# Kernel tuning notes

Measured on AMD Instinct MI355X. Metric: run time of the kernel, lower is better.

## Reference

```python
import jax, jax.numpy as jnp
import numpy as np

CAP = 15.0
EPS = 1e-6
NUM_HEADS = 16
HEAD_DIM = 64

def _rmsnorm(x, w):
    xf = x.astype(jnp.float32)
    var = jnp.mean(xf * xf, axis=-1, keepdims=True)
    return w * (xf * jax.lax.rsqrt(var + EPS)).astype(x.dtype)

def _gate(g):
    # sigmoid(soft_cap(g)) with cap 15
    return jax.nn.sigmoid(CAP * jnp.tanh(g / CAP))

def setup_inputs() -> dict:
    key = jax.random.key(0)
    ks = jax.random.split(key, 4)
    B, S, D = 4, 2048, 1024
    H, Dh = NUM_HEADS, HEAD_DIM
    return {
        "x": jax.random.normal(ks[0], (B, S, D), jnp.float32),
        "hidden_state": jnp.zeros((B, H, Dh, Dh), jnp.float32),
        "w_rms": jnp.ones((D,), jnp.float32),
        "w_qkv": jax.random.normal(ks[1], (D, 3 * H * Dh), jnp.float32) * 0.02,
        "w_gate": jax.random.normal(ks[2], (D, 3 * H), jnp.float32) * 0.02,
        "w_out": jax.random.normal(ks[3], (D, D), jnp.float32) * 0.02,
    }

def reference(x, hidden_state, w_rms, w_qkv, w_gate, w_out):
    B, S, D = x.shape
    H, Dh = NUM_HEADS, HEAD_DIM
    residual = x
    xn = _rmsnorm(x, w_rms)
    qkv = (xn @ w_qkv).reshape(B, S, 3, H, Dh)
    q, k, v = qkv[:, :, 0], qkv[:, :, 1], qkv[:, :, 2]  # [B,S,H,Dh]
    gates = _gate((xn @ w_gate).reshape(B, S, 3, H))
    i_g, f_g, o_g = gates[:, :, 0], gates[:, :, 1], gates[:, :, 2]  # [B,S,H]

    # time-major for scan: [S,B,H,...]
    def tm(a):
        return jnp.moveaxis(a, 1, 0)

    def step(state, inp):
        qt, kt, vt, it, ft, ot = inp  # [B,H,Dh]/[B,H]
        kv = kt[..., :, None] * vt[..., None, :]            # [B,H,Dh,Dh]
        state = ft[..., None, None] * state + it[..., None, None] * kv
        h = jnp.einsum('bhd,bhde->bhe', qt, state) * ot[..., None]
        return state, h

    _, h_seq = jax.lax.scan(step, hidden_state,
                            (tm(q), tm(k), tm(v), tm(i_g), tm(f_g), tm(o_g)))
    out = jnp.moveaxis(h_seq, 0, 1).reshape(B, S, H * Dh) @ w_out
    return residual + out
```

## Files before the change

### kernel.cpp

```cpp
#include <hip/hip_runtime.h>
#include <math.h>

typedef unsigned short u16;
typedef unsigned int   u32;
typedef __bf16 bf16x8 __attribute__((ext_vector_type(8)));
typedef float  f32x4  __attribute__((ext_vector_type(4)));

#define NBATCH 4
#define SEQ    2048
#define DIM    1024
#define NH     16
#define BH     64
#define NC     32
#define ROWS   8192
#define N1     3200

__device__ __forceinline__ u16 f2bf(float f) {
  u32 u = __builtin_bit_cast(u32, f);
  u32 r = u + 0x7fffu + ((u >> 16) & 1u);
  return (u16)(r >> 16);
}
__device__ __forceinline__ float bf2f(u16 h) {
  return __builtin_bit_cast(float, (u32)h << 16);
}

__device__ __forceinline__ void gl2lds16(const u16* g, u16* l) {
  __builtin_amdgcn_global_load_lds(
      (const __attribute__((address_space(1))) u32*)g,
      (__attribute__((address_space(3))) u32*)l, 16, 0, 0);
}

__global__ __launch_bounds__(256) void transpose_w(const float* __restrict__ W,
                                                   u16* __restrict__ Bt, int K, int N) {
  __shared__ float tile[32][33];
  const int n0 = blockIdx.x * 32, k0 = blockIdx.y * 32;
  const int tx = threadIdx.x, ty = threadIdx.y;
  #pragma unroll
  for (int i = 0; i < 4; i++)
    tile[ty + i * 8][tx] = W[(size_t)(k0 + ty + i * 8) * N + n0 + tx];
  __syncthreads();
  #pragma unroll
  for (int i = 0; i < 4; i++)
    Bt[(size_t)(n0 + ty + i * 8) * K + k0 + tx] = f2bf(tile[tx][ty + i * 8]);
}

__global__ __launch_bounds__(256) void fill_gateW(const float* __restrict__ wg,
                                                  u16* __restrict__ Bt) {
  const int g = blockIdx.x;
  const int tid = threadIdx.x;
  #pragma unroll
  for (int kk = 0; kk < 4; kk++) {
    const int k = kk * 256 + tid;
    u16 v = 0;
    if (g < 48) v = f2bf(wg[(size_t)k * 48 + g]);
    Bt[(size_t)(3072 + g) * 1024 + k] = v;
  }
}

__global__ __launch_bounds__(256) void rmsnorm_k(const float* __restrict__ x,
                                                 const float* __restrict__ w,
                                                 u16* __restrict__ xn) {
  const int row = blockIdx.x, tid = threadIdx.x;
  const float4 xv = *(const float4*)&x[(size_t)row * 1024 + tid * 4];
  float ss = xv.x * xv.x + xv.y * xv.y + xv.z * xv.z + xv.w * xv.w;
  #pragma unroll
  for (int off = 32; off > 0; off >>= 1) ss += __shfl_down(ss, off);
  __shared__ float red[4];
  if ((tid & 63) == 0) red[tid >> 6] = ss;
  __syncthreads();
  const float tot = red[0] + red[1] + red[2] + red[3];
  const float scale = rsqrtf(tot * (1.0f / 1024.0f) + 1e-6f);
  const float4 wv = *(const float4*)&w[tid * 4];
  const u16 o0 = f2bf(xv.x * scale * wv.x), o1 = f2bf(xv.y * scale * wv.y);
  const u16 o2 = f2bf(xv.z * scale * wv.z), o3 = f2bf(xv.w * scale * wv.w);
  uint2 ov;
  ov.x = (u32)o0 | ((u32)o1 << 16);
  ov.y = (u32)o2 | ((u32)o3 << 16);
  *(uint2*)&xn[(size_t)row * 1024 + tid * 4] = ov;
}

__device__ __forceinline__ void gemm_core(const u16* __restrict__ A, const u16* __restrict__ Bt,
                                          int K, int rowBase, int colBase,
                                          u16* As, u16* Bs, f32x4 (&acc)[4][4]) {
  const int tid = threadIdx.x;
  const int lane = tid & 63, wave = tid >> 6;
  const int q = lane >> 4, m16 = lane & 15;
  const int wm = wave & 1, wn = wave >> 1;
  const int srow = wave * 16 + (lane >> 2);
  const int scol = (lane & 3) * 8;
  const u16* gA0 = &A [(size_t)(rowBase + srow) * K + scol];
  const u16* gA1 = gA0 + (size_t)64 * K;
  const u16* gB0 = &Bt[(size_t)(colBase + srow) * K + scol];
  const u16* gB1 = gB0 + (size_t)64 * K;
  u16* lA0 = As + wave * 512 + lane * 8;
  u16* lA1 = lA0 + 2048;
  u16* lB0 = Bs + wave * 512 + lane * 8;
  u16* lB1 = lB0 + 2048;
  for (int kb = 0; kb < K / 32; ++kb) {
    __syncthreads();
    gl2lds16(gA0, lA0);
    gl2lds16(gA1, lA1);
    gl2lds16(gB0, lB0);
    gl2lds16(gB1, lB1);
    gA0 += 32; gA1 += 32; gB0 += 32; gB1 += 32;
    __syncthreads();
    bf16x8 af[4], bfr[4];
    #pragma unroll
    for (int mi = 0; mi < 4; mi++)
      af[mi] = *(const bf16x8*)&As[(wm * 64 + mi * 16 + m16) * 32 + q * 8];
    #pragma unroll
    for (int ni = 0; ni < 4; ni++)
      bfr[ni] = *(const bf16x8*)&Bs[(wn * 64 + ni * 16 + m16) * 32 + q * 8];
    #pragma unroll
    for (int mi = 0; mi < 4; mi++)
      #pragma unroll
      for (int ni = 0; ni < 4; ni++)
        acc[mi][ni] = __builtin_amdgcn_mfma_f32_16x16x32_bf16(af[mi], bfr[ni], acc[mi][ni], 0, 0, 0);
  }
}

__global__ __launch_bounds__(256) void gemm_qkv(const u16* __restrict__ A, const u16* __restrict__ Bt,
                                                u16* __restrict__ Qb, u16* __restrict__ Kb,
                                                u16* __restrict__ Vb, float* __restrict__ gates) {
  __shared__ __attribute__((aligned(16))) u16 As[128 * 32];
  __shared__ __attribute__((aligned(16))) u16 Bs[128 * 32];
  f32x4 acc[4][4] = {};
  const int rowBase = blockIdx.x * 128, colBase = blockIdx.y * 128;
  gemm_core(A, Bt, 1024, rowBase, colBase, As, Bs, acc);
  const int tid = threadIdx.x;
  const int lane = tid & 63, wave = tid >> 6;
  const int q = lane >> 4, m16 = lane & 15;
  const int wm = wave & 1, wn = wave >> 1;
  #pragma unroll
  for (int ni = 0; ni < 4; ni++) {
    const int gcol = colBase + wn * 64 + ni * 16 + m16;
    #pragma unroll
    for (int mi = 0; mi < 4; mi++) {
      #pragma unroll
      for (int r = 0; r < 4; r++) {
        const int grow = rowBase + wm * 64 + mi * 16 + q * 4 + r;
        const float v = acc[mi][ni][r];
        const int b = grow >> 11, t = grow & 2047;
        if (gcol < 3072) {
          const int which = gcol >> 10, rem = gcol & 1023;
          const int h = rem >> 6, d = rem & 63;
          u16* dst = (which == 0) ? Qb : ((which == 1) ? Kb : Vb);
          dst[(((size_t)(b * 16 + h)) * 2048 + t) * 64 + d] = f2bf(v);
        } else if (gcol < 3120) {
          const int c2 = gcol - 3072, which = c2 >> 4, hh = c2 & 15;
          const float g = 1.0f / (1.0f + expf(-(15.0f * tanhf(v * (1.0f / 15.0f)))));
          gates[((size_t)which * 64 + (b * 16 + hh)) * 2048 + t] = g;
        }
      }
    }
  }
}

__global__ __launch_bounds__(256) void gemm_out(const u16* __restrict__ A, const u16* __restrict__ Bt,
                                                const float* __restrict__ resid,
                                                float* __restrict__ out) {
  __shared__ __attribute__((aligned(16))) u16 As[128 * 32];
  __shared__ __attribute__((aligned(16))) u16 Bs[128 * 32];
  f32x4 acc[4][4] = {};
  const int rowBase = blockIdx.x * 128, colBase = blockIdx.y * 128;
  gemm_core(A, Bt, 1024, rowBase, colBase, As, Bs, acc);
  const int tid = threadIdx.x;
  const int lane = tid & 63, wave = tid >> 6;
  const int q = lane >> 4, m16 = lane & 15;
  const int wm = wave & 1, wn = wave >> 1;
  #pragma unroll
  for (int mi = 0; mi < 4; mi++)
    #pragma unroll
    for (int ni = 0; ni < 4; ni++)
      #pragma unroll
      for (int r = 0; r < 4; r++) {
        const int grow = rowBase + wm * 64 + mi * 16 + q * 4 + r;
        const int gcol = colBase + wn * 64 + ni * 16 + m16;
        const size_t idx = (size_t)grow * 1024 + gcol;
        out[idx] = acc[mi][ni][r] + resid[idx];
      }
}

__global__ __launch_bounds__(64) void la_k(const float* __restrict__ gates,
                                           float* __restrict__ la) {
  const int bh = blockIdx.x >> 5, c = blockIdx.x & 31, lane = threadIdx.x;
  const int t = c * 64 + lane;
  float x = logf(gates[(size_t)(64 + bh) * 2048 + t]);
  #pragma unroll
  for (int off = 1; off < 64; off <<= 1) {
    const float y = __shfl_up(x, off);
    if (lane >= off) x += y;
  }
  la[(size_t)bh * 2048 + t] = x;
}

__global__ __launch_bounds__(256) void passA_k(const u16* __restrict__ Qb, const u16* __restrict__ Kb,
                                               const u16* __restrict__ Vb,
                                               const float* __restrict__ gates,
                                               const float* __restrict__ la,
                                               float* __restrict__ Mbuf, u16* __restrict__ hseq) {
  __shared__ u16 Ql[64][72], Kl[64][72], KTl[64][72], VTl[64][72], Pl[64][72];
  __shared__ float laS[64], iS[64];
  const int tid = threadIdx.x;
  const int bh = blockIdx.x >> 5, c = blockIdx.x & 31;
  const int lane = tid & 63, w = tid >> 6;
  const int q = lane >> 4, m16 = lane & 15;
  const size_t base = ((size_t)bh * 2048 + c * 64) * 64;
  const int tbase = bh * 2048 + c * 64;

  {
    const int s = tid >> 2, db = (tid & 3) * 16;
    if (tid < 64) {
      laS[tid] = la[tbase + tid];
      iS[tid] = gates[(size_t)bh * 2048 + c * 64 + tid];
    }
    const float la_s = la[tbase + s];
    const float i_s = gates[(size_t)bh * 2048 + c * 64 + s];
    const float la63 = la[tbase + 63];
    const float wk = expf(la63 - la_s) * i_s;
    const uint4 q0 = *(const uint4*)&Qb[base + s * 64 + db];
    const uint4 q1 = *(const uint4*)&Qb[base + s * 64 + db + 8];
    *(uint4*)&Ql[s][db] = q0;
    *(uint4*)&Ql[s][db + 8] = q1;
    const uint4 k0 = *(const uint4*)&Kb[base + s * 64 + db];
    const uint4 k1 = *(const uint4*)&Kb[base + s * 64 + db + 8];
    *(uint4*)&Kl[s][db] = k0;
    *(uint4*)&Kl[s][db + 8] = k1;
    u16 ktmp[16];
    *(uint4*)&ktmp[0] = k0;
    *(uint4*)&ktmp[8] = k1;
    #pragma unroll
    for (int j = 0; j < 16; j++) KTl[db + j][s] = f2bf(wk * bf2f(ktmp[j]));
    const uint4 v0 = *(const uint4*)&Vb[base + s * 64 + db];
    const uint4 v1 = *(const uint4*)&Vb[base + s * 64 + db + 8];
    u16 vtmp[16];
    *(uint4*)&vtmp[0] = v0;
    *(uint4*)&vtmp[8] = v1;
    #pragma unroll
    for (int j = 0; j < 16; j++) VTl[db + j][s] = vtmp[j];
  }
  __syncthreads();

  f32x4 pacc[4] = {};
  #pragma unroll
  for (int ks = 0; ks < 2; ks++) {
    const bf16x8 aq = *(const bf16x8*)&Ql[w * 16 + m16][ks * 32 + q * 8];
    #pragma unroll
    for (int ni = 0; ni < 4; ni++) {
      const bf16x8 bk = *(const bf16x8*)&Kl[ni * 16 + m16][ks * 32 + q * 8];
      pacc[ni] = __builtin_amdgcn_mfma_f32_16x16x32_bf16(aq, bk, pacc[ni], 0, 0, 0);
    }
  }
  #pragma unroll
  for (int ni = 0; ni < 4; ni++)
    #pragma unroll
    for (int r = 0; r < 4; r++) {
      const int tt = w * 16 + q * 4 + r, ss = ni * 16 + m16;
      float Wts = 0.0f;
      if (ss <= tt) Wts = expf(laS[tt] - laS[ss]) * iS[ss];
      Pl[tt][ss] = f2bf(pacc[ni][r] * Wts);
    }
  __syncthreads();

  f32x4 hacc[4] = {}, macc[4] = {};
  #pragma unroll
  for (int ks = 0; ks < 2; ks++) {
    const bf16x8 ap = *(const bf16x8*)&Pl[w * 16 + m16][ks * 32 + q * 8];
    const bf16x8 ak = *(const bf16x8*)&KTl[w * 16 + m16][ks * 32 + q * 8];
    #pragma unroll
    for (int ni = 0; ni < 4; ni++) {
      const bf16x8 bv = *(const bf16x8*)&VTl[ni * 16 + m16][ks * 32 + q * 8];
      hacc[ni] = __builtin_amdgcn_mfma_f32_16x16x32_bf16(ap, bv, hacc[ni], 0, 0, 0);
      macc[ni] = __builtin_amdgcn_mfma_f32_16x16x32_bf16(ak, bv, macc[ni], 0, 0, 0);
    }
  }
  const int b = bh >> 4, h = bh & 15;
  #pragma unroll
  for (int ni = 0; ni < 4; ni++)
    #pragma unroll
    for (int r = 0; r < 4; r++) {
      const int tt = w * 16 + q * 4 + r, e = ni * 16 + m16;
      const int tg = c * 64 + tt;
      hseq[((size_t)b * 2048 + tg) * 1024 + h * 64 + e] = f2bf(hacc[ni][r]);
      Mbuf[(((size_t)bh * 32 + c) * 64 + tt) * 64 + e] = macc[ni][r];
    }
}

__global__ __launch_bounds__(256) void passB_k(float* __restrict__ Mbuf,
                                               const float* __restrict__ hidden,
                                               const float* __restrict__ la) {
  const int bh = blockIdx.x >> 4;
  const int e = (blockIdx.x & 15) * 256 + threadIdx.x;
  __shared__ float Gs[32];
  if (threadIdx.x < 32)
    Gs[threadIdx.x] = expf(la[(size_t)bh * 2048 + threadIdx.x * 64 + 63]);
  __syncthreads();
  float st = hidden[(size_t)bh * 4096 + e];
  float* M = &Mbuf[(size_t)bh * 32 * 4096 + e];
  float m_next = M[0];
  #pragma unroll 4
  for (int c = 0; c < 32; c++) {
    const float m_cur = m_next;
    if (c < 31) m_next = M[(size_t)(c + 1) * 4096];
    M[(size_t)c * 4096] = st;
    st = Gs[c] * st + m_cur;
  }
}

__global__ __launch_bounds__(256) void passC_k(const u16* __restrict__ Qb,
                                               const float* __restrict__ Sprev,
                                               const float* __restrict__ la,
                                               const float* __restrict__ gates,
                                               u16* __restrict__ hseq) {
  __shared__ u16 aQl[64][72], STl[64][72];
  const int tid = threadIdx.x;
  const int bh = blockIdx.x >> 5, c = blockIdx.x & 31;
  const int lane = tid & 63, w = tid >> 6;
  const int q = lane >> 4, m16 = lane & 15;
  const size_t base = ((size_t)bh * 2048 + c * 64) * 64;
  const int tbase = bh * 2048 + c * 64;
  {
    const int s = tid >> 2, db = (tid & 3) * 16;
    const float a_s = expf(la[tbase + s]);
    const uint4 q0 = *(const uint4*)&Qb[base + s * 64 + db];
    const uint4 q1 = *(const uint4*)&Qb[base + s * 64 + db + 8];
    u16 qtmp[16];
    *(uint4*)&qtmp[0] = q0;
    *(uint4*)&qtmp[8] = q1;
    #pragma unroll
    for (int j = 0; j < 16; j++) aQl[s][db + j] = f2bf(a_s * bf2f(qtmp[j]));
    const float* Sp = &Sprev[((size_t)bh * 32 + c) * 4096];
    #pragma unroll
    for (int j = 0; j < 16; j++) STl[db + j][s] = f2bf(Sp[s * 64 + db + j]);
  }
  __syncthreads();
  f32x4 acc[4] = {};
  #pragma unroll
  for (int ks = 0; ks < 2; ks++) {
    const bf16x8 a = *(const bf16x8*)&aQl[w * 16 + m16][ks * 32 + q * 8];
    #pragma unroll
    for (int ni = 0; ni < 4; ni++) {
      const bf16x8 bb = *(const bf16x8*)&STl[ni * 16 + m16][ks * 32 + q * 8];
      acc[ni] = __builtin_amdgcn_mfma_f32_16x16x32_bf16(a, bb, acc[ni], 0, 0, 0);
    }
  }
  const int b = bh >> 4, h = bh & 15;
  #pragma unroll
  for (int ni = 0; ni < 4; ni++)
    #pragma unroll
    for (int r = 0; r < 4; r++) {
      const int tt = w * 16 + q * 4 + r, e = ni * 16 + m16;
      const int tg = c * 64 + tt;
      const float o = gates[(size_t)(128 + bh) * 2048 + tg];
      const size_t idx = ((size_t)b * 2048 + tg) * 1024 + h * 64 + e;
      hseq[idx] = f2bf(o * (bf2f(hseq[idx]) + acc[ni][r]));
    }
}

extern "C" void kernel_launch(void* const* d_in, const int* in_sizes, int n_in,
                              void* d_out, int out_size, void* d_ws, size_t ws_size,
                              hipStream_t stream) {
  (void)in_sizes; (void)n_in; (void)out_size; (void)ws_size;
  const float* x      = (const float*)d_in[0];
  const float* hidden = (const float*)d_in[1];
  const float* w_rms  = (const float*)d_in[2];
  const float* w_qkv  = (const float*)d_in[3];
  const float* w_gate = (const float*)d_in[4];
  const float* w_out  = (const float*)d_in[5];
  float* out = (float*)d_out;

  char* p = (char*)d_ws;
  u16* wqkvT = (u16*)p;  p += (size_t)N1 * 1024 * 2;
  u16* woutT = (u16*)p;  p += (size_t)1024 * 1024 * 2;
  u16* xn    = (u16*)p;  p += (size_t)ROWS * 1024 * 2;
  u16* Qb    = (u16*)p;  p += (size_t)BH * 2048 * 64 * 2;
  u16* Kb    = (u16*)p;  p += (size_t)BH * 2048 * 64 * 2;
  u16* Vb    = (u16*)p;  p += (size_t)BH * 2048 * 64 * 2;
  float* gates = (float*)p; p += (size_t)3 * BH * 2048 * 4;
  float* la    = (float*)p; p += (size_t)BH * 2048 * 4;
  float* Mbuf  = (float*)p; p += (size_t)BH * NC * 4096 * 4;
  u16* hseq  = (u16*)p;  p += (size_t)ROWS * 1024 * 2;

  transpose_w<<<dim3(96, 32), dim3(32, 8), 0, stream>>>(w_qkv, wqkvT, 1024, 3072);
  transpose_w<<<dim3(32, 32), dim3(32, 8), 0, stream>>>(w_out, woutT, 1024, 1024);
  fill_gateW<<<128, 256, 0, stream>>>(w_gate, wqkvT);
  rmsnorm_k<<<ROWS, 256, 0, stream>>>(x, w_rms, xn);
  gemm_qkv<<<dim3(64, 25), 256, 0, stream>>>(xn, wqkvT, Qb, Kb, Vb, gates);
  la_k<<<BH * NC, 64, 0, stream>>>(gates, la);
  passA_k<<<BH * NC, 256, 0, stream>>>(Qb, Kb, Vb, gates, la, Mbuf, hseq);
  passB_k<<<BH * 16, 256, 0, stream>>>(Mbuf, hidden, la);
  passC_k<<<BH * NC, 256, 0, stream>>>(Qb, Mbuf, la, gates, hseq);
  gemm_out<<<dim3(64, 8), 256, 0, stream>>>(hseq, woutT, x, out);
}
```

Measured before the change: 277.4 us.

## Use 256x128 GEMM tiles with 8 waves and LDS-staged coalesced QKV stores

Both GEMMs move from 128x128 tiles with 4 waves to 256x128 tiles with 8 waves, so each B tile loaded into LDS is reused across twice as many rows and the grid has half as many blocks. The QKV epilogue now writes bf16 results into per-wave LDS scratch and then stores 16-byte vectors per row into the head-major Q/K/V buffers, replacing scattered 2-byte writes. Gate columns keep the old per-element path. Fewer blocks may reduce occupancy or leave the wave count on the CUs unbalanced, and the larger block raises register and LDS pressure.

```diff
diff --git a/kernel.cpp b/kernel.cpp
--- a/kernel.cpp
+++ b/kernel.cpp
@@ -79,30 +79,29 @@
   *(uint2*)&xn[(size_t)row * 1024 + tid * 4] = ov;
 }
 
-__device__ __forceinline__ void gemm_core(const u16* __restrict__ A, const u16* __restrict__ Bt,
-                                          int K, int rowBase, int colBase,
-                                          u16* As, u16* Bs, f32x4 (&acc)[4][4]) {
-  const int tid = threadIdx.x;
-  const int lane = tid & 63, wave = tid >> 6;
+__device__ __forceinline__ void gemm_core256(const u16* __restrict__ A, const u16* __restrict__ Bt,
+                                             int K, int rowBase, int colBase,
+                                             u16* As, u16* Bs, f32x4 (&acc)[4][4]) {
+  const int tid = threadIdx.x;
+  const int lane = tid & 63;
   const int q = lane >> 4, m16 = lane & 15;
-  const int wm = wave & 1, wn = wave >> 1;
-  const int srow = wave * 16 + (lane >> 2);
-  const int scol = (lane & 3) * 8;
-  const u16* gA0 = &A [(size_t)(rowBase + srow) * K + scol];
-  const u16* gA1 = gA0 + (size_t)64 * K;
-  const u16* gB0 = &Bt[(size_t)(colBase + srow) * K + scol];
-  const u16* gB1 = gB0 + (size_t)64 * K;
-  u16* lA0 = As + wave * 512 + lane * 8;
-  u16* lA1 = lA0 + 2048;
-  u16* lB0 = Bs + wave * 512 + lane * 8;
-  u16* lB1 = lB0 + 2048;
+  const int wave = tid >> 6;
+  const int wm = wave & 3, wn = wave >> 2;
+  const int cA0 = tid;
+  const int cA1 = tid + 512;
+  const int cB  = tid;
+  const u16* gA0 = &A [(size_t)(rowBase + (cA0 >> 2)) * K + (cA0 & 3) * 8];
+  const u16* gA1 = &A [(size_t)(rowBase + (cA1 >> 2)) * K + (cA1 & 3) * 8];
+  const u16* gB  = &Bt[(size_t)(colBase + (cB  >> 2)) * K + (cB  & 3) * 8];
+  u16* lA0 = As + cA0 * 8;
+  u16* lA1 = As + cA1 * 8;
+  u16* lB  = Bs + cB * 8;
   for (int kb = 0; kb < K / 32; ++kb) {
     __syncthreads();
     gl2lds16(gA0, lA0);
     gl2lds16(gA1, lA1);
-    gl2lds16(gB0, lB0);
-    gl2lds16(gB1, lB1);
-    gA0 += 32; gA1 += 32; gB0 += 32; gB1 += 32;
+    gl2lds16(gB,  lB);
+    gA0 += 32; gA1 += 32; gB += 32;
     __syncthreads();
     bf16x8 af[4], bfr[4];
     #pragma unroll
@@ -119,55 +118,74 @@
   }
 }
 
-__global__ __launch_bounds__(256) void gemm_qkv(const u16* __restrict__ A, const u16* __restrict__ Bt,
-                                                u16* __restrict__ Qb, u16* __restrict__ Kb,
-                                                u16* __restrict__ Vb, float* __restrict__ gates) {
-  __shared__ __attribute__((aligned(16))) u16 As[128 * 32];
+__global__ __launch_bounds__(512, 4) void gemm_qkv(const u16* __restrict__ A, const u16* __restrict__ Bt,
+                                                   u16* __restrict__ Qb, u16* __restrict__ Kb,
+                                                   u16* __restrict__ Vb, float* __restrict__ gates) {
+  __shared__ __attribute__((aligned(16))) u16 As[256 * 32];
   __shared__ __attribute__((aligned(16))) u16 Bs[128 * 32];
   f32x4 acc[4][4] = {};
-  const int rowBase = blockIdx.x * 128, colBase = blockIdx.y * 128;
-  gemm_core(A, Bt, 1024, rowBase, colBase, As, Bs, acc);
+  const int rowBase = blockIdx.x * 256, colBase = blockIdx.y * 128;
+  gemm_core256(A, Bt, 1024, rowBase, colBase, As, Bs, acc);
   const int tid = threadIdx.x;
   const int lane = tid & 63, wave = tid >> 6;
   const int q = lane >> 4, m16 = lane & 15;
-  const int wm = wave & 1, wn = wave >> 1;
-  #pragma unroll
-  for (int ni = 0; ni < 4; ni++) {
-    const int gcol = colBase + wn * 64 + ni * 16 + m16;
+  const int wm = wave & 3, wn = wave >> 2;
+  __syncthreads();
+  if (colBase < 3072) {
+    const int which = colBase >> 10;
+    u16* dstBase = (which == 0) ? Qb : ((which == 1) ? Kb : Vb);
+    const int b = rowBase >> 11;
+    const int h = ((colBase & 1023) >> 6) + wn;
+    const int tRow0 = (rowBase & 2047) + wm * 64;
+    u16* scratch = As + wave * 1024;
+    u16* headBase = dstBase + ((size_t)(b * 16 + h)) * 2048 * 64;
+    const int rr = lane >> 2, co = (lane & 3) * 16;
     #pragma unroll
     for (int mi = 0; mi < 4; mi++) {
       #pragma unroll
-      for (int r = 0; r < 4; r++) {
-        const int grow = rowBase + wm * 64 + mi * 16 + q * 4 + r;
-        const float v = acc[mi][ni][r];
-        const int b = grow >> 11, t = grow & 2047;
-        if (gcol < 3072) {
-          const int which = gcol >> 10, rem = gcol & 1023;
-          const int h = rem >> 6, d = rem & 63;
-          u16* dst = (which == 0) ? Qb : ((which == 1) ? Kb : Vb);
-          dst[(((size_t)(b * 16 + h)) * 2048 + t) * 64 + d] = f2bf(v);
-        } else if (gcol < 3120) {
-          const int c2 = gcol - 3072, which = c2 >> 4, hh = c2 & 15;
-          const float g = 1.0f / (1.0f + expf(-(15.0f * tanhf(v * (1.0f / 15.0f)))));
-          gates[((size_t)which * 64 + (b * 16 + hh)) * 2048 + t] = g;
-        }
+      for (int ni = 0; ni < 4; ni++)
+        #pragma unroll
+        for (int r = 0; r < 4; r++)
+          scratch[(q * 4 + r) * 64 + ni * 16 + m16] = f2bf(acc[mi][ni][r]);
+      const uint4 d0 = *(const uint4*)&scratch[rr * 64 + co];
+      const uint4 d1 = *(const uint4*)&scratch[rr * 64 + co + 8];
+      u16* gp = headBase + (size_t)(tRow0 + mi * 16 + rr) * 64 + co;
+      *(uint4*)gp = d0;
+      *(uint4*)(gp + 8) = d1;
+    }
+  } else {
+    #pragma unroll
+    for (int ni = 0; ni < 4; ni++) {
+      const int c2 = wn * 64 + ni * 16 + m16;
+      if (c2 < 48) {
+        const int which = c2 >> 4, hh = c2 & 15;
+        #pragma unroll
+        for (int mi = 0; mi < 4; mi++)
+          #pragma unroll
+          for (int r = 0; r < 4; r++) {
+            const int grow = rowBase + wm * 64 + mi * 16 + q * 4 + r;
+            const int b = grow >> 11, t = grow & 2047;
+            const float v = acc[mi][ni][r];
+            const float g = 1.0f / (1.0f + expf(-(15.0f * tanhf(v * (1.0f / 15.0f)))));
+            gates[((size_t)which * 64 + (b * 16 + hh)) * 2048 + t] = g;
+          }
       }
     }
   }
 }
 
-__global__ __launch_bounds__(256) void gemm_out(const u16* __restrict__ A, const u16* __restrict__ Bt,
-                                                const float* __restrict__ resid,
-                                                float* __restrict__ out) {
-  __shared__ __attribute__((aligned(16))) u16 As[128 * 32];
+__global__ __launch_bounds__(512, 4) void gemm_out(const u16* __restrict__ A, const u16* __restrict__ Bt,
+                                                   const float* __restrict__ resid,
+                                                   float* __restrict__ out) {
+  __shared__ __attribute__((aligned(16))) u16 As[256 * 32];
   __shared__ __attribute__((aligned(16))) u16 Bs[128 * 32];
   f32x4 acc[4][4] = {};
-  const int rowBase = blockIdx.x * 128, colBase = blockIdx.y * 128;
-  gemm_core(A, Bt, 1024, rowBase, colBase, As, Bs, acc);
+  const int rowBase = blockIdx.x * 256, colBase = blockIdx.y * 128;
+  gemm_core256(A, Bt, 1024, rowBase, colBase, As, Bs, acc);
   const int tid = threadIdx.x;
   const int lane = tid & 63, wave = tid >> 6;
   const int q = lane >> 4, m16 = lane & 15;
-  const int wm = wave & 1, wn = wave >> 1;
+  const int wm = wave & 3, wn = wave >> 2;
   #pragma unroll
   for (int mi = 0; mi < 4; mi++)
     #pragma unroll
@@ -385,10 +403,10 @@
   transpose_w<<<dim3(32, 32), dim3(32, 8), 0, stream>>>(w_out, woutT, 1024, 1024);
   fill_gateW<<<128, 256, 0, stream>>>(w_gate, wqkvT);
   rmsnorm_k<<<ROWS, 256, 0, stream>>>(x, w_rms, xn);
-  gemm_qkv<<<dim3(64, 25), 256, 0, stream>>>(xn, wqkvT, Qb, Kb, Vb, gates);
+  gemm_qkv<<<dim3(32, 25), 512, 0, stream>>>(xn, wqkvT, Qb, Kb, Vb, gates);
   la_k<<<BH * NC, 64, 0, stream>>>(gates, la);
   passA_k<<<BH * NC, 256, 0, stream>>>(Qb, Kb, Vb, gates, la, Mbuf, hseq);
   passB_k<<<BH * 16, 256, 0, stream>>>(Mbuf, hidden, la);
   passC_k<<<BH * NC, 256, 0, stream>>>(Qb, Mbuf, la, gates, hseq);
-  gemm_out<<<dim3(64, 8), 256, 0, stream>>>(hseq, woutT, x, out);
-}
+  gemm_out<<<dim3(32, 8), 512, 0, stream>>>(hseq, woutT, x, out);
+}
```

After: 272.0 us. Within noise of the previous version (-1.9%).
